# Kernel tuning notes

Measured on AMD Instinct MI355X. Metric: run time of the kernel, lower is better.

The kernel has to match this reference:

```python
import jax, jax.numpy as jnp
import numpy as np

# ---- static config (matches init_kwargs) ----
B = 8            # batch_size (graphs)
N = 10000        # num_nodes per graph
NTOT = B * N     # total node rows (80000)
E = 320000       # edges (only over first N nodes, as in the original code)
D = 128          # input_dim == backbone_channels (shared conv forces equality)
H = 4            # heads
C = 128          # backbone_channels (per-head out dim, concat=False)
L = 3            # num_backbone_layers
K = 30           # sort-pool k
HID = 512        # mlp_hidden_dim
OUT = 2          # output_dim
EXPECTED = K * L * C * H + 1  # buggy mlp_input_dim from __init__ -> zero-pad
BN_EPS = 1e-5


def setup_inputs() -> dict:
    key = jax.random.key(0)
    ks = jax.random.split(key, 20)
    s = 1.0 / np.sqrt(D)
    inp = {
        "x": jax.random.normal(ks[0], (NTOT, D), dtype=jnp.float32),
        "edge_index": jax.random.randint(ks[1], (2, E), 0, N, dtype=jnp.int32),
        "age": jax.random.normal(ks[2], (B,), dtype=jnp.float32),
        # shared TransformerConv params (reused across all L layers)
        "Wq": jax.random.normal(ks[3], (D, H * C), dtype=jnp.float32) * s,
        "bq": jax.random.normal(ks[4], (H * C,), dtype=jnp.float32) * 0.02,
        "Wk": jax.random.normal(ks[5], (D, H * C), dtype=jnp.float32) * s,
        "bk": jax.random.normal(ks[6], (H * C,), dtype=jnp.float32) * 0.02,
        "Wv": jax.random.normal(ks[7], (D, H * C), dtype=jnp.float32) * s,
        "bv": jax.random.normal(ks[8], (H * C,), dtype=jnp.float32) * 0.02,
        "Wskip": jax.random.normal(ks[9], (D, C), dtype=jnp.float32) * s,
        "bskip": jax.random.normal(ks[10], (C,), dtype=jnp.float32) * 0.02,
        # per-layer BatchNorm (eval mode: running stats)
        "bn_gamma": 1.0 + 0.1 * jax.random.normal(ks[11], (L, C), dtype=jnp.float32),
        "bn_beta": 0.1 * jax.random.normal(ks[12], (L, C), dtype=jnp.float32),
        "bn_mean": 0.1 * jax.random.normal(ks[13], (L, C), dtype=jnp.float32),
        "bn_var": jax.random.uniform(ks[14], (L, C), dtype=jnp.float32, minval=0.5, maxval=1.5),
        # MLP head (2 layers: EXPECTED->HID, ReLU, HID->OUT)
        "W1": jax.random.normal(ks[15], (EXPECTED, HID), dtype=jnp.float32) * (1.0 / np.sqrt(EXPECTED)),
        "b1": jnp.zeros((HID,), dtype=jnp.float32),
        "W2": jax.random.normal(ks[16], (HID, OUT), dtype=jnp.float32) * (1.0 / np.sqrt(HID)),
        "b2": jnp.zeros((OUT,), dtype=jnp.float32),
    }
    return inp


def _transformer_conv(h, src, dst, Wq, bq, Wk, bk, Wv, bv, Wskip, bskip):
    # PyG TransformerConv, concat=False, root_weight=True, eval (no attn dropout)
    q = (h @ Wq + bq).reshape(NTOT, H, C)
    k = (h @ Wk + bk).reshape(NTOT, H, C)
    v = (h @ Wv + bv).reshape(NTOT, H, C)
    # per-edge attention logits [E, H]
    alpha = jnp.einsum("ehc,ehc->eh", q[dst], k[src]) / np.sqrt(C).astype(np.float32)
    # segment softmax over incoming edges of each target node
    m = jax.ops.segment_max(alpha, dst, num_segments=NTOT)          # [NTOT, H]
    e = jnp.exp(alpha - m[dst])
    denom = jax.ops.segment_sum(e, dst, num_segments=NTOT)          # [NTOT, H]
    a = e / (denom[dst] + 1e-16)                                    # [E, H]
    out = jax.ops.segment_sum(a[:, :, None] * v[src], dst, num_segments=NTOT)  # [NTOT,H,C]
    return out.mean(axis=1) + h @ Wskip + bskip                     # concat=False -> head mean


def reference(x, edge_index, age, Wq, bq, Wk, bk, Wv, bv, Wskip, bskip,
              bn_gamma, bn_beta, bn_mean, bn_var, W1, b1, W2, b2):
    src, dst = edge_index[0], edge_index[1]
    h = x
    feats = []
    for i in range(L):  # fixed small layer count; shared conv weights
        h = _transformer_conv(h, src, dst, Wq, bq, Wk, bk, Wv, bv, Wskip, bskip)
        h = (h - bn_mean[i]) * (bn_gamma[i] / jnp.sqrt(bn_var[i] + BN_EPS)) + bn_beta[i]
        h = jax.nn.relu(h)  # dropout: eval mode no-op
        feats.append(h)
    h = feats[-1]  # concat_input_graph=False
    # global_sort_pool: sort nodes per graph by last channel (desc), take top-k
    xr = h.reshape(B, N, C)
    idx = jnp.argsort(-xr[:, :, -1], axis=1)[:, :K]                 # [B, K]
    pooled = jnp.take_along_axis(xr, idx[:, :, None], axis=1)       # [B, K, C]
    z = pooled.reshape(B, K * C)
    z = jnp.concatenate([z, age.reshape(B, 1)], axis=1)             # [B, K*C+1]
    # zero-pad to the (mismatched) expected MLP input dim, as in the original
    z = jnp.concatenate([z, jnp.zeros((B, EXPECTED - z.shape[1]), dtype=z.dtype)], axis=1)
    z = jax.nn.relu(z @ W1 + b1)
    z = z @ W2 + b2
    return jax.nn.log_softmax(z, axis=-1)
```

## Files before the change

### kernel.cpp

```cpp
#include <hip/hip_runtime.h>
#include <cmath>


#define NN    10000
#define NTOT  80000
#define EE    320000
#define CH    128

__device__ __forceinline__ float rl_f(float v, int lane) {
    return __uint_as_float(__builtin_amdgcn_readlane(__float_as_uint(v), lane));
}

__global__ __launch_bounds__(256) void precompute_kernel(
    const float* __restrict__ Wq, const float* __restrict__ bq,
    const float* __restrict__ Wk, const float* __restrict__ Wv,
    const float* __restrict__ bv, const float* __restrict__ Wskip,
    const float* __restrict__ bskip,
    const float* __restrict__ bn_gamma, const float* __restrict__ bn_beta,
    const float* __restrict__ bn_mean, const float* __restrict__ bn_var,
    float* __restrict__ Bcat, float* __restrict__ biascat,
    float* __restrict__ Wcomb, float* __restrict__ bvbar,
    float* __restrict__ bnS, float* __restrict__ bnB)
{
    const float inv_sqrtC = 0.08838834764831845f;
    int idx = blockIdx.x * 256 + threadIdx.x;
    if (idx < 65536) {
        int c = idx >> 9;
        int o = idx & 511;
        int hbase = o & ~127;
        int j = o & 127;
        const float* wq = Wq + c * 512 + hbase;
        const float* wk = Wk + j * 512 + hbase;
        float s = 0.f;
        for (int cc = 0; cc < 128; cc++) s = fmaf(wq[cc], wk[cc], s);
        Bcat[c * 640 + o] = s * inv_sqrtC;
        return;
    }
    idx -= 65536;
    if (idx < 16384) {
        int c = idx >> 7, n = idx & 127;
        Bcat[c * 640 + 512 + n] = Wskip[c * 128 + n];
        return;
    }
    idx -= 16384;
    if (idx < 512) {
        int o = idx, hbase = o & ~127, j = o & 127;
        const float* wk = Wk + j * 512 + hbase;
        const float* bqp = bq + hbase;
        float s = 0.f;
        for (int cc = 0; cc < 128; cc++) s = fmaf(bqp[cc], wk[cc], s);
        biascat[o] = s * inv_sqrtC;
        return;
    }
    idx -= 512;
    if (idx < 128) {
        biascat[512 + idx] = bskip[idx];
        return;
    }
    idx -= 128;
    if (idx < 65536) {
        int k = idx >> 7;
        int n = idx & 127;
        int h = k >> 7, c = k & 127;
        Wcomb[k * 128 + n] = Wv[c * 512 + h * 128 + n] * 0.25f;
        return;
    }
    idx -= 65536;
    if (idx < 128) {
        float s = 0.f;
        for (int h = 0; h < 4; h++) s += bv[h * 128 + idx];
        bvbar[idx] = 0.25f * s;
        return;
    }
    idx -= 128;
    if (idx < 384) {
        float sc = bn_gamma[idx] / sqrtf(bn_var[idx] + 1e-5f);
        bnS[idx] = sc;
        bnB[idx] = bn_beta[idx] - bn_mean[idx] * sc;
        return;
    }
}

__global__ void count_kernel(const int* __restrict__ dst, int* __restrict__ deg) {
    int e = blockIdx.x * 256 + threadIdx.x;
    if (e < EE) atomicAdd(&deg[dst[e]], 1);
}

__global__ __launch_bounds__(1024) void scan_kernel(const int* __restrict__ deg,
                                                    int* __restrict__ rowstart) {
    __shared__ int part[1024];
    const int t = threadIdx.x;
    int loc[10];
    int s = 0;
    for (int i = 0; i < 10; i++) {
        int idx = t * 10 + i;
        int v = (idx < NN) ? deg[idx] : 0;
        loc[i] = s; s += v;
    }
    part[t] = s; __syncthreads();
    for (int d = 1; d < 1024; d <<= 1) {
        int v = (t >= d) ? part[t - d] : 0;
        __syncthreads();
        part[t] += v;
        __syncthreads();
    }
    int base = (t == 0) ? 0 : part[t - 1];
    for (int i = 0; i < 10; i++) {
        int idx = t * 10 + i;
        if (idx <= NN) rowstart[idx] = base + loc[i];
    }
}

__global__ void scatter_kernel(const int* __restrict__ src, const int* __restrict__ dst,
                               const int* __restrict__ rowstart, int* __restrict__ cursor,
                               int* __restrict__ csr_src) {
    int e = blockIdx.x * 256 + threadIdx.x;
    if (e < EE) {
        int d = dst[e];
        int p = atomicAdd(&cursor[d], 1);
        csr_src[rowstart[d] + p] = src[e];
    }
}

__global__ __launch_bounds__(256) void skip3_kernel(
    const float* __restrict__ xup,
    const float* __restrict__ Wskip,
    const float* __restrict__ bskip,
    const float* __restrict__ bnS, const float* __restrict__ bnB,
    float* __restrict__ h3up)
{
    __shared__ float rowb[64][132];
    __shared__ float Bs[16][132];
    const int t = threadIdx.x;
    const int r0 = blockIdx.x * 64;
    const int Mrem = min(64, (NTOT - NN) - r0);
    const int tx = t & 15;
    const int ty = t >> 4;

    for (int f = t; f < 64 * 32; f += 256) {
        int row = f >> 5, c4 = (f & 31) * 4;
        if (row < Mrem)
            *(float4*)&rowb[row][c4] = *(const float4*)(xup + (size_t)(r0 + row) * CH + c4);
    }

    for (int l = 0; l < 3; l++) {
        float acc[4][8];
        #pragma unroll
        for (int i = 0; i < 4; i++)
            #pragma unroll
            for (int j = 0; j < 8; j++) acc[i][j] = 0.f;

        for (int k0 = 0; k0 < 128; k0 += 16) {
            __syncthreads();
            for (int f = t; f < 512; f += 256) {
                int kk = f >> 5, n4 = (f & 31) * 4;
                *(float4*)&Bs[kk][n4] = *(const float4*)(Wskip + (size_t)(k0 + kk) * 128 + n4);
            }
            __syncthreads();
            #pragma unroll
            for (int kk = 0; kk < 16; kk++) {
                const float4 b0 = *(const float4*)&Bs[kk][tx * 8];
                const float4 b1 = *(const float4*)&Bs[kk][tx * 8 + 4];
                const float bf[8] = {b0.x, b0.y, b0.z, b0.w, b1.x, b1.y, b1.z, b1.w};
                #pragma unroll
                for (int i = 0; i < 4; i++) {
                    const float af = rowb[ty * 4 + i][k0 + kk];
                    #pragma unroll
                    for (int j = 0; j < 8; j++)
                        acc[i][j] = fmaf(af, bf[j], acc[i][j]);
                }
            }
        }
        __syncthreads();
        const float* bS = bnS + l * 128;
        const float* bB = bnB + l * 128;
        #pragma unroll
        for (int i = 0; i < 4; i++) {
            const int row = ty * 4 + i;
            #pragma unroll
            for (int j = 0; j < 8; j++) {
                const int n = tx * 8 + j;
                float xv = acc[i][j] + bskip[n];
                xv = fmaf(xv, bS[n], bB[n]);
                rowb[row][n] = fmaxf(xv, 0.f);
            }
        }
    }
    __syncthreads();
    for (int f = t; f < 64 * 32; f += 256) {
        int row = f >> 5, c4 = (f & 31) * 4;
        if (row < Mrem)
            *(float4*)(h3up + (size_t)(r0 + row) * CH + c4) = *(const float4*)&rowb[row][c4];
    }
}

template<int BM, int BN, int TM, int TN, int MODE>
__global__ __launch_bounds__(256) void gemm_fp32(
    const float* __restrict__ A, int lda,
    const float* __restrict__ B, int ldb,
    const float* __restrict__ bias, const float* __restrict__ bias2,
    const int* __restrict__ deg,
    const float* __restrict__ Cold,
    const float* __restrict__ bnS, const float* __restrict__ bnB,
    float* __restrict__ C0, int ldc0,
    float* __restrict__ C1, int ldc1,
    int M, int K)
{
    constexpr int BK = 16;
    __shared__ float As[BK][BM + 4];
    __shared__ float Bs[BK][BN + 4];
    const int t  = threadIdx.x;
    const int tx = t % (BN / TN);
    const int ty = t / (BN / TN);
    const int m0 = blockIdx.x * BM;
    const int n0 = blockIdx.y * BN;
    float acc[TM][TN];
    #pragma unroll
    for (int i = 0; i < TM; i++)
        #pragma unroll
        for (int j = 0; j < TN; j++) acc[i][j] = 0.f;

    for (int k0 = 0; k0 < K; k0 += BK) {
        #pragma unroll
        for (int f = t; f < BM * 4; f += 256) {
            int row = f >> 2, fc = f & 3;
            int gm = m0 + row;
            float4 v = make_float4(0.f, 0.f, 0.f, 0.f);
            if (gm < M) v = *(const float4*)(A + (size_t)gm * lda + k0 + fc * 4);
            As[fc * 4 + 0][row] = v.x;
            As[fc * 4 + 1][row] = v.y;
            As[fc * 4 + 2][row] = v.z;
            As[fc * 4 + 3][row] = v.w;
        }
        #pragma unroll
        for (int f = t; f < BK * (BN / 4); f += 256) {
            int kk = f / (BN / 4);
            int nn = (f % (BN / 4)) * 4;
            *(float4*)(&Bs[kk][nn]) = *(const float4*)(B + (size_t)(k0 + kk) * ldb + n0 + nn);
        }
        __syncthreads();
        #pragma unroll
        for (int kk = 0; kk < BK; kk++) {
            float af[TM], bf[TN];
            if constexpr (TM == 2) {
                float2 v = *(const float2*)&As[kk][ty * 2];
                af[0] = v.x; af[1] = v.y;
            } else {
                #pragma unroll
                for (int ii = 0; ii < TM; ii += 4) {
                    float4 v = *(const float4*)&As[kk][ty * TM + ii];
                    af[ii + 0] = v.x; af[ii + 1] = v.y; af[ii + 2] = v.z; af[ii + 3] = v.w;
                }
            }
            #pragma unroll
            for (int jj = 0; jj < TN; jj += 4) {
                float4 v = *(const float4*)&Bs[kk][tx * TN + jj];
                bf[jj + 0] = v.x; bf[jj + 1] = v.y; bf[jj + 2] = v.z; bf[jj + 3] = v.w;
            }
            #pragma unroll
            for (int i = 0; i < TM; i++)
                #pragma unroll
                for (int j = 0; j < TN; j++)
                    acc[i][j] = fmaf(af[i], bf[j], acc[i][j]);
        }
        __syncthreads();
    }
    #pragma unroll
    for (int i = 0; i < TM; i++) {
        int gm = m0 + ty * TM + i;
        if (gm >= M) continue;
        const bool addB2 = (MODE == 4) ? (deg[gm] > 0) : false;
        #pragma unroll
        for (int j = 0; j < TN; j += 4) {
            const int nb = n0 + tx * TN + j;
            float4 v;
            float* vp = &v.x;
            if (MODE == 4) {
                const float4 old = *(const float4*)(Cold + (size_t)gm * ldc1 + nb);
                const float* op = &old.x;
                #pragma unroll
                for (int q = 0; q < 4; q++) {
                    const int n = nb + q;
                    float x = acc[i][j + q] + op[q];
                    if (addB2) x += bias2[n];
                    x = fmaf(x, bnS[n], bnB[n]);
                    vp[q] = fmaxf(x, 0.f);
                }
                *(float4*)(C0 + (size_t)gm * ldc0 + nb) = v;
            } else {
                #pragma unroll
                for (int q = 0; q < 4; q++)
                    vp[q] = acc[i][j + q] + bias[nb + q];
                if (nb < 512)
                    *(float4*)(C0 + (size_t)gm * ldc0 + nb) = v;
                else
                    *(float4*)(C1 + (size_t)gm * ldc1 + nb - 512) = v;
            }
        }
    }
}

__global__ __launch_bounds__(256) void attn_kernel(
    const float* __restrict__ h,
    const float* __restrict__ u,
    float* __restrict__ g,
    const int* __restrict__ rowstart,
    const int* __restrict__ csr_src)
{
    __shared__ float h_lds[128 * 65];
    __shared__ __align__(16) float palpha[4 * 64 * 4];
    __shared__ __align__(16) float wT[64 * 4];
    __shared__ __align__(16) float scale_lds[4];
    __shared__ __align__(16) float s_lds[4];
    __shared__ __align__(16) float merge[128 * 4];
    __shared__ int src_lds[64];

    const int n  = blockIdx.x;
    const int t  = threadIdx.x;
    const int w  = t >> 6;
    const int l  = t & 63;
    const int c  = t & 127;
    const int jh = t >> 7;
    const int rs   = rowstart[n];
    const int degn = rowstart[n + 1] - rs;

    if (degn == 0) {
        g[(size_t)n * 512 + t] = 0.f;
        g[(size_t)n * 512 + 256 + t] = 0.f;
        return;
    }
    float u_reg0 = u[(size_t)n * 512 + ((l >> 5)) * 128 + 32 * w + (l & 31)];
    float u_reg1 = u[(size_t)n * 512 + ((l >> 5) + 2) * 128 + 32 * w + (l & 31)];

    float m_run = -INFINITY, s_run = 0.f;
    float4 acc4 = make_float4(0.f, 0.f, 0.f, 0.f);

    for (int base = 0; base < degn; base += 64) {
        const int len = min(64, degn - base);
        __syncthreads();
        if (t < len) src_lds[t] = csr_src[rs + base + t];
        __syncthreads();
        for (int f = t; f < len * 32; f += 256) {
            const int j = f >> 5, c4 = (f & 31) * 4;
            const float4 v = *(const float4*)(h + (size_t)src_lds[j] * CH + c4);
            h_lds[(c4 + 0) * 65 + j] = v.x;
            h_lds[(c4 + 1) * 65 + j] = v.y;
            h_lds[(c4 + 2) * 65 + j] = v.z;
            h_lds[(c4 + 3) * 65 + j] = v.w;
        }
        __syncthreads();
        {
            float p0 = 0.f, p1 = 0.f, p2 = 0.f, p3 = 0.f;
            #pragma unroll
            for (int dc = 0; dc < 32; dc++) {
                const float hv = h_lds[(32 * w + dc) * 65 + l];
                p0 = fmaf(rl_f(u_reg0, dc),      hv, p0);
                p1 = fmaf(rl_f(u_reg0, 32 + dc), hv, p1);
                p2 = fmaf(rl_f(u_reg1, dc),      hv, p2);
                p3 = fmaf(rl_f(u_reg1, 32 + dc), hv, p3);
            }
            palpha[(0 * 64 + l) * 4 + w] = p0;
            palpha[(1 * 64 + l) * 4 + w] = p1;
            palpha[(2 * 64 + l) * 4 + w] = p2;
            palpha[(3 * 64 + l) * 4 + w] = p3;
        }
        __syncthreads();
        {
            const float4 pa = *(const float4*)&palpha[(w * 64 + l) * 4];
            float alpha = (l < len) ? (pa.x + pa.y + pa.z + pa.w) : -INFINITY;
            float mx = alpha;
            #pragma unroll
            for (int d = 1; d < 64; d <<= 1) mx = fmaxf(mx, __shfl_xor(mx, d, 64));
            const float newm = fmaxf(m_run, mx);
            float e = (l < len) ? __expf(alpha - newm) : 0.f;
            float ss = e;
            #pragma unroll
            for (int d = 1; d < 64; d <<= 1) ss += __shfl_xor(ss, d, 64);
            const float sc = (m_run == -INFINITY) ? 0.f : __expf(m_run - newm);
            s_run = s_run * sc + ss;
            m_run = newm;
            wT[l * 4 + w] = e;
            if (l == 0) scale_lds[w] = sc;
        }
        __syncthreads();
        {
            const float4 scv = *(const float4*)scale_lds;
            acc4.x *= scv.x; acc4.y *= scv.y; acc4.z *= scv.z; acc4.w *= scv.w;
            const int j0 = jh * 32;
            const int j1 = min(len, j0 + 32);
            for (int j = j0; j < j1; j++) {
                const float hv = h_lds[c * 65 + j];
                const float4 wv = *(const float4*)&wT[j * 4];
                acc4.x = fmaf(wv.x, hv, acc4.x);
                acc4.y = fmaf(wv.y, hv, acc4.y);
                acc4.z = fmaf(wv.z, hv, acc4.z);
                acc4.w = fmaf(wv.w, hv, acc4.w);
            }
        }
    }
    if (l == 0) s_lds[w] = s_run;
    __syncthreads();
    if (jh == 1) *(float4*)&merge[c * 4] = acc4;
    __syncthreads();
    if (jh == 0) {
        const float4 o  = *(const float4*)&merge[c * 4];
        const float4 sv = *(const float4*)s_lds;
        g[(size_t)n * 512 + 0 * 128 + c] = (acc4.x + o.x) / (sv.x + 1e-16f);
        g[(size_t)n * 512 + 1 * 128 + c] = (acc4.y + o.y) / (sv.y + 1e-16f);
        g[(size_t)n * 512 + 2 * 128 + c] = (acc4.z + o.z) / (sv.z + 1e-16f);
        g[(size_t)n * 512 + 3 * 128 + c] = (acc4.w + o.w) / (sv.w + 1e-16f);
    }
}

__global__ __launch_bounds__(256) void radix_pool_kernel(
    const float* __restrict__ h3, const float* __restrict__ age,
    float* __restrict__ z)
{
    __shared__ unsigned int keys[NN];
    __shared__ int hist[256];
    __shared__ int sbuf[256];
    __shared__ unsigned int sel_prefix;
    __shared__ int sel_need;
    __shared__ int gt_counter;
    __shared__ unsigned int cand_key[30];
    __shared__ int cand_idx[30];
    __shared__ int order[30];

    const int b = blockIdx.x;
    const int t = threadIdx.x;

    for (int i = t; i < NN; i += 256)
        keys[i] = __float_as_uint(h3[((size_t)b * NN + i) * CH + 127]);
    if (t == 0) { sel_prefix = 0u; sel_need = 30; gt_counter = 0; }
    __syncthreads();

    for (int r = 3; r >= 0; r--) {
        hist[t] = 0;
        __syncthreads();
        const int shift = r * 8;
        const unsigned int pmask = (r == 3) ? 0u : (0xFFFFFFFFu << ((r + 1) * 8));
        const unsigned int pref = sel_prefix;
        const int need = sel_need;
        for (int i = t; i < NN; i += 256) {
            unsigned int k = keys[i];
            if ((k & pmask) == pref)
                atomicAdd(&hist[(k >> shift) & 255u], 1);
        }
        __syncthreads();
        sbuf[t] = hist[255 - t];
        __syncthreads();
        for (int d = 1; d < 256; d <<= 1) {
            int o = (t >= d) ? sbuf[t - d] : 0;
            __syncthreads();
            sbuf[t] += o;
            __syncthreads();
        }
        {
            const int v = t;
            const int ge = sbuf[255 - v];
            const int gt = ge - hist[v];
            if (gt < need && need <= ge) {
                sel_prefix = pref | ((unsigned int)v << shift);
                sel_need = need - gt;
            }
        }
        __syncthreads();
    }

    const unsigned int T = sel_prefix;
    const int need_eq = sel_need;
    const int n_gt = 30 - need_eq;

    for (int i = t; i < NN; i += 256) {
        unsigned int k = keys[i];
        if (k > T) {
            int p = atomicAdd(&gt_counter, 1);
            cand_key[p] = k; cand_idx[p] = i;
        }
    }
    {
        const int CHK = (NN + 255) / 256;
        const int i0 = t * CHK, i1 = min(NN, i0 + CHK);
        int local = 0;
        for (int i = i0; i < i1; i++) if (keys[i] == T) local++;
        sbuf[t] = local;
        __syncthreads();
        for (int d = 1; d < 256; d <<= 1) {
            int o = (t >= d) ? sbuf[t - d] : 0;
            __syncthreads();
            sbuf[t] += o;
            __syncthreads();
        }
        int rank = (t == 0) ? 0 : sbuf[t - 1];
        for (int i = i0; i < i1; i++) {
            if (keys[i] == T) {
                if (rank < need_eq) { cand_key[n_gt + rank] = T; cand_idx[n_gt + rank] = i; }
                rank++;
            }
        }
    }
    __syncthreads();
    if (t < 30) {
        const unsigned int mk = cand_key[t];
        const int mi = cand_idx[t];
        int rk = 0;
        for (int j = 0; j < 30; j++) {
            const unsigned int ok = cand_key[j];
            const int oi = cand_idx[j];
            if (ok > mk || (ok == mk && oi < mi)) rk++;
        }
        order[rk] = t;
    }
    __syncthreads();
    for (int f = t; f < 30 * CH; f += 256) {
        int kk = f >> 7, cc = f & 127;
        z[(size_t)b * 3841 + f] = h3[((size_t)b * NN + cand_idx[order[kk]]) * CH + cc];
    }
    if (t == 0) z[(size_t)b * 3841 + 3840] = age[b];
}

__global__ __launch_bounds__(256) void mlp1_kernel(
    const float* __restrict__ z, const float* __restrict__ W1,
    float* __restrict__ zh)
{
    __shared__ float zs[256];
    const int b  = blockIdx.x >> 4;
    const int ic = blockIdx.x & 15;
    const int t  = threadIdx.x;
    const int i0 = ic * 241;
    const int i1 = min(3841, i0 + 241);
    float a0 = 0.f, a1 = 0.f;
    for (int cb = i0; cb < i1; cb += 256) {
        int cl = min(256, i1 - cb);
        __syncthreads();
        if (t < cl) zs[t] = z[(size_t)b * 3841 + cb + t];
        __syncthreads();
        #pragma unroll 4
        for (int q = 0; q < cl; q++) {
            float zv = zs[q];
            const float* wp = W1 + (size_t)(cb + q) * 512;
            a0 = fmaf(zv, wp[t], a0);
            a1 = fmaf(zv, wp[t + 256], a1);
        }
    }
    atomicAdd(&zh[(size_t)b * 512 + t], a0);
    atomicAdd(&zh[(size_t)b * 512 + t + 256], a1);
}

__global__ __launch_bounds__(256) void mlp2_kernel(
    const float* __restrict__ zh, const float* __restrict__ b1,
    const float* __restrict__ W2, const float* __restrict__ b2,
    float* __restrict__ out)
{
    __shared__ float r0[256], r1[256];
    const int b = blockIdx.x;
    const int t = threadIdx.x;
    float a0 = 0.f, a1 = 0.f;
    for (int j = t; j < 512; j += 256) {
        float v = fmaxf(zh[(size_t)b * 512 + j] + b1[j], 0.f);
        a0 = fmaf(v, W2[j * 2 + 0], a0);
        a1 = fmaf(v, W2[j * 2 + 1], a1);
    }
    r0[t] = a0; r1[t] = a1; __syncthreads();
    for (int s = 128; s > 0; s >>= 1) {
        if (t < s) { r0[t] += r0[t + s]; r1[t] += r1[t + s]; }
        __syncthreads();
    }
    if (t == 0) {
        float l0 = r0[0] + b2[0], l1 = r1[0] + b2[1];
        float m = fmaxf(l0, l1);
        float lse = m + logf(__expf(l0 - m) + __expf(l1 - m));
        out[b * 2 + 0] = l0 - lse;
        out[b * 2 + 1] = l1 - lse;
    }
}

extern "C" void kernel_launch(void* const* d_in, const int* in_sizes, int n_in,
                              void* d_out, int out_size, void* d_ws, size_t ws_size,
                              hipStream_t stream) {
    const float* x     = (const float*)d_in[0];
    const int*   ei    = (const int*)d_in[1];
    const float* age   = (const float*)d_in[2];
    const float* Wq    = (const float*)d_in[3];
    const float* bq    = (const float*)d_in[4];
    const float* Wk    = (const float*)d_in[5];
    const float* Wv    = (const float*)d_in[7];
    const float* bv    = (const float*)d_in[8];
    const float* Wskip = (const float*)d_in[9];
    const float* bskip = (const float*)d_in[10];
    const float* bn_g  = (const float*)d_in[11];
    const float* bn_b  = (const float*)d_in[12];
    const float* bn_m  = (const float*)d_in[13];
    const float* bn_v  = (const float*)d_in[14];
    const float* W1    = (const float*)d_in[15];
    const float* b1    = (const float*)d_in[16];
    const float* W2    = (const float*)d_in[17];
    const float* b2    = (const float*)d_in[18];

    float* ws = (float*)d_ws;
    float* h3      = ws;
    float* hlowA   = h3 + 10240000;
    float* hlowB   = hlowA + 1280000;
    float* u       = hlowB + 1280000;
    float* skipraw = u + 5120000;
    float* Bcat    = skipraw + 1280000;
    float* biascat = Bcat + 81920;
    float* Wcomb   = biascat + 640;
    float* bvbar   = Wcomb + 65536;
    float* bnS     = bvbar + 128;
    float* bnB     = bnS + 384;
    float* zbuf    = bnB + 384;
    float* zh      = zbuf + 30728;
    int* deg      = (int*)(zh + 4096);
    int* cursor   = deg + NN;
    int* rowstart = cursor + NN;
    int* csr_src  = rowstart + NN + 1;

    const int* srcI = ei;
    const int* dstI = ei + EE;

    hipMemsetAsync(deg, 0, sizeof(int) * (2 * NN), stream);
    hipMemsetAsync(zh, 0, sizeof(float) * 4096, stream);

    precompute_kernel<<<581, 256, 0, stream>>>(Wq, bq, Wk, Wv, bv, Wskip, bskip,
                                               bn_g, bn_b, bn_m, bn_v,
                                               Bcat, biascat, Wcomb, bvbar, bnS, bnB);
    count_kernel<<<1250, 256, 0, stream>>>(dstI, deg);
    scan_kernel<<<1, 1024, 0, stream>>>(deg, rowstart);
    scatter_kernel<<<1250, 256, 0, stream>>>(srcI, dstI, rowstart, cursor, csr_src);

    skip3_kernel<<<1094, 256, 0, stream>>>(x + (size_t)NN * CH, Wskip, bskip,
                                           bnS, bnB, h3 + (size_t)NN * CH);

    const float* hcur = x;
    for (int l = 0; l < 3; l++) {
        float* dest = (l == 0) ? hlowA : (l == 1) ? hlowB : h3;
        gemm_fp32<64, 64, 4, 4, 0><<<dim3(157, 10), 256, 0, stream>>>(
            hcur, CH, Bcat, 640, biascat, nullptr, nullptr, nullptr,
            nullptr, nullptr, u, 512, skipraw, CH, NN, 128);
        attn_kernel<<<NN, 256, 0, stream>>>(hcur, u, u, rowstart, csr_src);
        gemm_fp32<32, 64, 2, 4, 4><<<dim3(313, 2), 256, 0, stream>>>(
            u, 512, Wcomb, CH, nullptr, bvbar, deg, skipraw,
            bnS + l * 128, bnB + l * 128, dest, CH, nullptr, CH, NN, 512);
        hcur = dest;
    }
    radix_pool_kernel<<<8, 256, 0, stream>>>(h3, age, zbuf);
    mlp1_kernel<<<128, 256, 0, stream>>>(zbuf, W1, zh);
    mlp2_kernel<<<8, 256, 0, stream>>>(zh, b1, W2, b2, (float*)d_out);
}
```

Baseline: 677.6 us.

## Compute only sort keys for third skip layer and recompute selected rows lazily

For nodes beyond the first graph, the skip-only path now runs two full 128x128 layers and computes only channel 127 of the third layer as the sort key. The full third-layer rows are recomputed only for the 30 selected nodes per graph in a new gather kernel. The last GEMM also writes its channel-127 keys into a compact array, so the radix pool reads contiguous keys instead of strided rows. This trades a third dense layer over 70000 rows for a small extra kernel launch and per-row dot products, with possible rounding differences between the key and the recomputed row.

New measurement: 623.0 us. 1.09x faster.

```diff
diff --git a/kernel.cpp b/kernel.cpp
--- a/kernel.cpp
+++ b/kernel.cpp
@@ -122,15 +122,17 @@
     }
 }
 
-__global__ __launch_bounds__(256) void skip3_kernel(
+__global__ __launch_bounds__(256) void skip2_keys_kernel(
     const float* __restrict__ xup,
     const float* __restrict__ Wskip,
     const float* __restrict__ bskip,
     const float* __restrict__ bnS, const float* __restrict__ bnB,
-    float* __restrict__ h3up)
+    float* __restrict__ h2up,
+    float* __restrict__ gkeys)
 {
     __shared__ float rowb[64][132];
     __shared__ float Bs[16][132];
+    __shared__ float sWc[128];
     const int t = threadIdx.x;
     const int r0 = blockIdx.x * 64;
     const int Mrem = min(64, (NTOT - NN) - r0);
@@ -142,8 +144,9 @@
         if (row < Mrem)
             *(float4*)&rowb[row][c4] = *(const float4*)(xup + (size_t)(r0 + row) * CH + c4);
     }
-
-    for (int l = 0; l < 3; l++) {
+    if (t < 128) sWc[t] = Wskip[t * 128 + 127];
+
+    for (int l = 0; l < 2; l++) {
         float acc[4][8];
         #pragma unroll
         for (int i = 0; i < 4; i++)
@@ -159,8 +162,8 @@
             __syncthreads();
             #pragma unroll
             for (int kk = 0; kk < 16; kk++) {
-                const float4 b0 = *(const float4*)&Bs[kk][tx * 8];
-                const float4 b1 = *(const float4*)&Bs[kk][tx * 8 + 4];
+                const float4 b0 = *(const float4*)&Bs[kk][tx * 4];
+                const float4 b1 = *(const float4*)&Bs[kk][64 + tx * 4];
                 const float bf[8] = {b0.x, b0.y, b0.z, b0.w, b1.x, b1.y, b1.z, b1.w};
                 #pragma unroll
                 for (int i = 0; i < 4; i++) {
@@ -177,20 +180,36 @@
         #pragma unroll
         for (int i = 0; i < 4; i++) {
             const int row = ty * 4 + i;
+            float4 v0, v1;
+            float* p0 = &v0.x;
+            float* p1 = &v1.x;
             #pragma unroll
-            for (int j = 0; j < 8; j++) {
-                const int n = tx * 8 + j;
-                float xv = acc[i][j] + bskip[n];
-                xv = fmaf(xv, bS[n], bB[n]);
-                rowb[row][n] = fmaxf(xv, 0.f);
-            }
+            for (int q = 0; q < 4; q++) {
+                const int n0c = tx * 4 + q;
+                float xv = acc[i][q] + bskip[n0c];
+                xv = fmaf(xv, bS[n0c], bB[n0c]);
+                p0[q] = fmaxf(xv, 0.f);
+                const int n1c = 64 + tx * 4 + q;
+                float yv = acc[i][4 + q] + bskip[n1c];
+                yv = fmaf(yv, bS[n1c], bB[n1c]);
+                p1[q] = fmaxf(yv, 0.f);
+            }
+            *(float4*)&rowb[row][tx * 4] = v0;
+            *(float4*)&rowb[row][64 + tx * 4] = v1;
         }
     }
     __syncthreads();
+    if (t < Mrem) {
+        float s = 0.f;
+        for (int k = 0; k < 128; k++) s = fmaf(rowb[t][k], sWc[k], s);
+        s += bskip[127];
+        s = fmaf(s, bnS[2 * 128 + 127], bnB[2 * 128 + 127]);
+        gkeys[NN + r0 + t] = fmaxf(s, 0.f);
+    }
     for (int f = t; f < 64 * 32; f += 256) {
         int row = f >> 5, c4 = (f & 31) * 4;
         if (row < Mrem)
-            *(float4*)(h3up + (size_t)(r0 + row) * CH + c4) = *(const float4*)&rowb[row][c4];
+            *(float4*)(h2up + (size_t)(r0 + row) * CH + c4) = *(const float4*)&rowb[row][c4];
     }
 }
 
@@ -204,7 +223,8 @@
     const float* __restrict__ bnS, const float* __restrict__ bnB,
     float* __restrict__ C0, int ldc0,
     float* __restrict__ C1, int ldc1,
-    int M, int K)
+    int M, int K,
+    float* __restrict__ keysOut)
 {
     constexpr int BK = 16;
     __shared__ float As[BK][BM + 4];
@@ -287,6 +307,7 @@
                     vp[q] = fmaxf(x, 0.f);
                 }
                 *(float4*)(C0 + (size_t)gm * ldc0 + nb) = v;
+                if (keysOut != nullptr && nb == 124) keysOut[gm] = v.w;
             } else {
                 #pragma unroll
                 for (int q = 0; q < 4; q++)
@@ -413,8 +434,8 @@
 }
 
 __global__ __launch_bounds__(256) void radix_pool_kernel(
-    const float* __restrict__ h3, const float* __restrict__ age,
-    float* __restrict__ z)
+    const float* __restrict__ gkeys, const float* __restrict__ age,
+    int* __restrict__ sel, float* __restrict__ z)
 {
     __shared__ unsigned int keys[NN];
     __shared__ int hist[256];
@@ -430,7 +451,7 @@
     const int t = threadIdx.x;
 
     for (int i = t; i < NN; i += 256)
-        keys[i] = __float_as_uint(h3[((size_t)b * NN + i) * CH + 127]);
+        keys[i] = __float_as_uint(gkeys[(size_t)b * NN + i]);
     if (t == 0) { sel_prefix = 0u; sel_need = 30; gt_counter = 0; }
     __syncthreads();
 
@@ -512,11 +533,37 @@
         order[rk] = t;
     }
     __syncthreads();
-    for (int f = t; f < 30 * CH; f += 256) {
-        int kk = f >> 7, cc = f & 127;
-        z[(size_t)b * 3841 + f] = h3[((size_t)b * NN + cand_idx[order[kk]]) * CH + cc];
-    }
+    if (t < 30) sel[b * 30 + t] = cand_idx[order[t]];
     if (t == 0) z[(size_t)b * 3841 + 3840] = age[b];
+}
+
+__global__ __launch_bounds__(128) void gather_kernel(
+    const float* __restrict__ h3,
+    const float* __restrict__ h2up,
+    const float* __restrict__ Wskip, const float* __restrict__ bskip,
+    const float* __restrict__ bnS, const float* __restrict__ bnB,
+    const int* __restrict__ sel, float* __restrict__ z)
+{
+    __shared__ float sh[128];
+    const int blk = blockIdx.x;
+    const int b = blk / 30;
+    const int kk = blk % 30;
+    const int c = threadIdx.x;
+    const int i = sel[b * 30 + kk];
+    const size_t g = (size_t)b * NN + i;
+    float v;
+    if (b == 0) {
+        v = h3[g * CH + c];
+    } else {
+        sh[c] = h2up[(g - NN) * CH + c];
+        __syncthreads();
+        float s = 0.f;
+        for (int k = 0; k < 128; k++) s = fmaf(sh[k], Wskip[k * 128 + c], s);
+        s += bskip[c];
+        s = fmaf(s, bnS[2 * 128 + c], bnB[2 * 128 + c]);
+        v = fmaxf(s, 0.f);
+    }
+    z[(size_t)b * 3841 + kk * CH + c] = v;
 }
 
 __global__ __launch_bounds__(256) void mlp1_kernel(
@@ -615,6 +662,8 @@
     int* cursor   = deg + NN;
     int* rowstart = cursor + NN;
     int* csr_src  = rowstart + NN + 1;
+    float* keysG  = (float*)(csr_src + EE);
+    int* sel      = (int*)(keysG + NTOT);
 
     const int* srcI = ei;
     const int* dstI = ei + EE;
@@ -629,22 +678,25 @@
     scan_kernel<<<1, 1024, 0, stream>>>(deg, rowstart);
     scatter_kernel<<<1250, 256, 0, stream>>>(srcI, dstI, rowstart, cursor, csr_src);
 
-    skip3_kernel<<<1094, 256, 0, stream>>>(x + (size_t)NN * CH, Wskip, bskip,
-                                           bnS, bnB, h3 + (size_t)NN * CH);
+    skip2_keys_kernel<<<1094, 256, 0, stream>>>(x + (size_t)NN * CH, Wskip, bskip,
+                                                bnS, bnB, h3 + (size_t)NN * CH, keysG);
 
     const float* hcur = x;
     for (int l = 0; l < 3; l++) {
         float* dest = (l == 0) ? hlowA : (l == 1) ? hlowB : h3;
         gemm_fp32<64, 64, 4, 4, 0><<<dim3(157, 10), 256, 0, stream>>>(
             hcur, CH, Bcat, 640, biascat, nullptr, nullptr, nullptr,
-            nullptr, nullptr, u, 512, skipraw, CH, NN, 128);
+            nullptr, nullptr, u, 512, skipraw, CH, NN, 128, nullptr);
         attn_kernel<<<NN, 256, 0, stream>>>(hcur, u, u, rowstart, csr_src);
         gemm_fp32<32, 64, 2, 4, 4><<<dim3(313, 2), 256, 0, stream>>>(
             u, 512, Wcomb, CH, nullptr, bvbar, deg, skipraw,
-            bnS + l * 128, bnB + l * 128, dest, CH, nullptr, CH, NN, 512);
+            bnS + l * 128, bnB + l * 128, dest, CH, nullptr, CH, NN, 512,
+            (l == 2) ? keysG : nullptr);
         hcur = dest;
     }
-    radix_pool_kernel<<<8, 256, 0, stream>>>(h3, age, zbuf);
+    radix_pool_kernel<<<8, 256, 0, stream>>>(keysG, age, sel, zbuf);
+    gather_kernel<<<240, 128, 0, stream>>>(h3, h3 + (size_t)NN * CH, Wskip, bskip,
+                                           bnS, bnB, sel, zbuf);
     mlp1_kernel<<<128, 256, 0, stream>>>(zbuf, W1, zh);
     mlp2_kernel<<<8, 256, 0, stream>>>(zh, b1, W2, b2, (float*)d_out);
 }
```
